# Kernel optimization log

Measured on AMD Instinct MI355X. Metric: run time of the kernel, lower is better.

The kernel has to match this reference:

```python
import jax, jax.numpy as jnp
import numpy as np

D_MODEL = 1024
NUM_HEADS = 16
HEAD_DIM = D_MODEL // NUM_HEADS
BATCH = 2048


def setup_inputs() -> dict:
    key = jax.random.key(0)
    ks = jax.random.split(key, 11)
    s = 1.0 / np.sqrt(D_MODEL)
    inp = {
        "q": jax.random.normal(ks[0], (BATCH, D_MODEL), jnp.float32),
        "k": jax.random.normal(ks[1], (BATCH, D_MODEL), jnp.float32),
        "v": jax.random.normal(ks[2], (BATCH, D_MODEL), jnp.float32),
        "Wq": jax.random.normal(ks[3], (D_MODEL, D_MODEL), jnp.float32) * s,
        "bq": jnp.zeros((D_MODEL,), jnp.float32),
        "Wk": jax.random.normal(ks[4], (D_MODEL, D_MODEL), jnp.float32) * s,
        "bk": jnp.zeros((D_MODEL,), jnp.float32),
        "Wv": jax.random.normal(ks[5], (D_MODEL, D_MODEL), jnp.float32) * s,
        "bv": jnp.zeros((D_MODEL,), jnp.float32),
        "Wo": jax.random.normal(ks[6], (D_MODEL, D_MODEL), jnp.float32) * s,
        "bo": jnp.zeros((D_MODEL,), jnp.float32),
    }
    return inp


def reference(q, k, v, Wq, bq, Wk, bk, Wv, bv, Wo, bo):
    b = q.shape[0]
    # linear projections (torch Linear: x @ W.T + b)
    qh = (q @ Wq.T + bq).reshape(b, NUM_HEADS, HEAD_DIM).transpose(1, 0, 2)  # (h, b, dh)
    kh = (k @ Wk.T + bk).reshape(b, NUM_HEADS, HEAD_DIM).transpose(1, 0, 2)  # (h, b, dh)
    # attention across the batch dimension: (h, b, b)
    scores = jnp.einsum('hid,hjd->hij', qh, kh) / jnp.sqrt(jnp.float32(HEAD_DIM))
    attn = jax.nn.softmax(scores, axis=-1)
    # pool_method == 'mean': v stays full-width, mean over heads
    vp = v @ Wv.T + bv                               # (b, d_model)
    out = jnp.einsum('hij,jd->hid', attn, vp)        # (h, b, d_model)
    out = out.mean(axis=0)                           # (b, d_model)
    out = out @ Wo.T + bo
    return out
```

## Files before the change

### kernel.cpp

```cpp
#include <hip/hip_runtime.h>
#include <hip/hip_bf16.h>
#include <stdint.h>

#define D_MODEL 1024
#define NUM_HEADS 16
#define HEAD_DIM 64
#define BATCH 2048

typedef unsigned short u16;
typedef __bf16 bf16x8 __attribute__((ext_vector_type(8)));
typedef float f32x4 __attribute__((ext_vector_type(4)));
typedef u16 u16x8 __attribute__((ext_vector_type(8)));

typedef __attribute__((address_space(1))) void gv_t;
typedef __attribute__((address_space(3))) void lv_t;

__device__ __forceinline__ u16 f2bf(float f) {
    uint32_t u = __builtin_bit_cast(uint32_t, f);
    return (u16)((u + 0x7fffu + ((u >> 16) & 1u)) >> 16);
}
__device__ __forceinline__ f32x4 fzero4() { f32x4 v = {0.f, 0.f, 0.f, 0.f}; return v; }

template<int N> __device__ __forceinline__ void waitv() {
    if constexpr (N == 0) asm volatile("s_waitcnt vmcnt(0)" ::: "memory");
    else if constexpr (N == 2) asm volatile("s_waitcnt vmcnt(2)" ::: "memory");
    else if constexpr (N == 4) asm volatile("s_waitcnt vmcnt(4)" ::: "memory");
    else if constexpr (N == 6) asm volatile("s_waitcnt vmcnt(6)" ::: "memory");
}
#define BAR() do { __builtin_amdgcn_s_barrier(); __builtin_amdgcn_sched_barrier(0); } while (0)

struct Conv7 {
    const float* src[7];
    u16* dst[7];
    int n[7];
};

__global__ __launch_bounds__(256) void convert_kernel(Conv7 a) {
    const int y = blockIdx.y;
    const int n = a.n[y];
    const long base = (long)(blockIdx.x * 256 + threadIdx.x) * 8;
    if (base >= n) return;
    const float* s = a.src[y] + base;
    const float4 f0 = *(const float4*)s;
    const float4 f1 = *(const float4*)(s + 4);
    u16x8 o;
    o[0] = f2bf(f0.x); o[1] = f2bf(f0.y); o[2] = f2bf(f0.z); o[3] = f2bf(f0.w);
    o[4] = f2bf(f1.x); o[5] = f2bf(f1.y); o[6] = f2bf(f1.z); o[7] = f2bf(f1.w);
    *(u16x8*)(a.dst[y] + base) = o;
}

struct G3 {
    const u16* A[3];
    const u16* Bt[3];
    const float* bias[3];
    void* C[3];
    int trans[3];
    int ldc[3];
};

__global__ __launch_bounds__(256, 3) void proj128_kernel(G3 g, int K) {
    __shared__ __align__(16) u16 As[3][128 * 32];
    __shared__ __align__(16) u16 Bs[3][128 * 32];
    const int z = blockIdx.z;
    const u16* __restrict__ A = g.A[z];
    const u16* __restrict__ Bt = g.Bt[z];
    const int tid = threadIdx.x, lane = tid & 63, wid = tid >> 6;
    const int l15 = lane & 15, l4 = lane >> 4;
    const int wr = wid >> 1, wc = wid & 1;
    const size_t brow = blockIdx.x, bcol = blockIdx.y;
    const int trow = tid >> 2;
    const int cswz = ((tid & 3) ^ (trow & 3)) * 8;
    const int sa = l15 & 3;

    const u16* Ag = A + (brow * 128 + trow) * (size_t)K + cswz;
    const u16* Bg = Bt + (bcol * 128 + trow) * (size_t)K + cswz;

    f32x4 acc[4][4];
#pragma unroll
    for (int m = 0; m < 4; m++)
#pragma unroll
        for (int n = 0; n < 4; n++) acc[m][n] = fzero4();

#define STGP(bi, k0) do { \
        __builtin_amdgcn_global_load_lds((gv_t*)(Ag + (k0)), (lv_t*)(&As[bi][tid * 8]), 16, 0, 0); \
        __builtin_amdgcn_global_load_lds((gv_t*)(Ag + (size_t)64 * K + (k0)), (lv_t*)(&As[bi][tid * 8 + 2048]), 16, 0, 0); \
        __builtin_amdgcn_global_load_lds((gv_t*)(Bg + (k0)), (lv_t*)(&Bs[bi][tid * 8]), 16, 0, 0); \
        __builtin_amdgcn_global_load_lds((gv_t*)(Bg + (size_t)64 * K + (k0)), (lv_t*)(&Bs[bi][tid * 8 + 2048]), 16, 0, 0); \
    } while (0)

    const int NT = K / 32;
    STGP(0, 0);
    STGP(1, 32);
    int cur = 0, pf = 2;
    for (int t = 0; t < NT; ++t) {
        if (t + 1 < NT) waitv<4>(); else waitv<0>();
        BAR();
        bf16x8 a[4], b[4];
#pragma unroll
        for (int m = 0; m < 4; m++) {
            const int row = wr * 64 + m * 16 + l15;
            a[m] = *(const bf16x8*)&As[cur][row * 32 + ((l4 ^ sa) * 8)];
        }
#pragma unroll
        for (int n = 0; n < 4; n++) {
            const int row = wc * 64 + n * 16 + l15;
            b[n] = *(const bf16x8*)&Bs[cur][row * 32 + ((l4 ^ sa) * 8)];
        }
        if (t + 2 < NT) STGP(pf, (t + 2) * 32);
        __builtin_amdgcn_s_setprio(1);
#pragma unroll
        for (int m = 0; m < 4; m++)
#pragma unroll
            for (int n = 0; n < 4; n++)
                acc[m][n] = __builtin_amdgcn_mfma_f32_16x16x32_bf16(a[m], b[n], acc[m][n], 0, 0, 0);
        __builtin_amdgcn_s_setprio(0);
        cur = (cur == 2) ? 0 : cur + 1;
        pf = (pf == 2) ? 0 : pf + 1;
    }
#undef STGP

    const int trans = g.trans[z];
    const size_t ldc = g.ldc[z];
    const float* bias = g.bias[z];
#pragma unroll
    for (int m = 0; m < 4; m++)
#pragma unroll
        for (int n = 0; n < 4; n++) {
            const size_t col = bcol * 128 + wc * 64 + n * 16 + l15;
            const float bv = bias[col];
#pragma unroll
            for (int j = 0; j < 4; j++) {
                const size_t row = brow * 128 + wr * 64 + m * 16 + l4 * 4 + j;
                const float val = acc[m][n][j] + bv;
                const size_t idx = trans ? (col * ldc + row) : (row * ldc + col);
                ((u16*)g.C[z])[idx] = f2bf(val);
            }
        }
}

template<int OUT_BF16, int HAS_BIAS>
__global__ __launch_bounds__(256, 2) void gemm64(G3 g, int K) {
    __shared__ __align__(16) u16 As[3][128 * 64];
    __shared__ __align__(16) u16 Bs[3][64 * 64];
    const int z = blockIdx.z;
    const u16* __restrict__ A = g.A[z];
    const u16* __restrict__ Bt = g.Bt[z];
    const int tid = threadIdx.x, lane = tid & 63, wid = tid >> 6;
    const int l15 = lane & 15, l4 = lane >> 4;
    const int wr = wid >> 1, wc = wid & 1;
    const size_t brow = blockIdx.x, bcol = blockIdx.y;
    const int trow = tid >> 3;
    const int cswz = ((tid & 7) ^ (trow & 7)) * 8;
    const int sa = l15 & 7;

    const u16* Ag = A + (brow * 128 + trow) * (size_t)K + cswz;
    const u16* Bg = Bt + (bcol * 64 + trow) * (size_t)K + cswz;

    f32x4 acc[4][2];
#pragma unroll
    for (int m = 0; m < 4; m++)
#pragma unroll
        for (int n = 0; n < 2; n++) acc[m][n] = fzero4();

#define STG64(bi, k0) do { \
        __builtin_amdgcn_global_load_lds((gv_t*)(Ag + (k0)), (lv_t*)(&As[bi][tid * 8]), 16, 0, 0); \
        __builtin_amdgcn_global_load_lds((gv_t*)(Ag + (size_t)32 * K + (k0)), (lv_t*)(&As[bi][tid * 8 + 2048]), 16, 0, 0); \
        __builtin_amdgcn_global_load_lds((gv_t*)(Ag + (size_t)64 * K + (k0)), (lv_t*)(&As[bi][tid * 8 + 4096]), 16, 0, 0); \
        __builtin_amdgcn_global_load_lds((gv_t*)(Ag + (size_t)96 * K + (k0)), (lv_t*)(&As[bi][tid * 8 + 6144]), 16, 0, 0); \
        __builtin_amdgcn_global_load_lds((gv_t*)(Bg + (k0)), (lv_t*)(&Bs[bi][tid * 8]), 16, 0, 0); \
        __builtin_amdgcn_global_load_lds((gv_t*)(Bg + (size_t)32 * K + (k0)), (lv_t*)(&Bs[bi][tid * 8 + 2048]), 16, 0, 0); \
    } while (0)

    const int NT = K / 64;
    STG64(0, 0);
    STG64(1, 64);
    int cur = 0, pf = 2;
    for (int t = 0; t < NT; ++t) {
        if (t + 1 < NT) waitv<6>(); else waitv<0>();
        BAR();
        bf16x8 a[4][2], b[2][2];
#pragma unroll
        for (int m = 0; m < 4; m++)
#pragma unroll
            for (int kk = 0; kk < 2; kk++)
                a[m][kk] = *(const bf16x8*)&As[cur][(wr * 64 + m * 16 + l15) * 64 + (((kk * 4 + l4) ^ sa) * 8)];
#pragma unroll
        for (int n = 0; n < 2; n++)
#pragma unroll
            for (int kk = 0; kk < 2; kk++)
                b[n][kk] = *(const bf16x8*)&Bs[cur][(wc * 32 + n * 16 + l15) * 64 + (((kk * 4 + l4) ^ sa) * 8)];
        if (t + 2 < NT) STG64(pf, (t + 2) * 64);
        __builtin_amdgcn_s_setprio(1);
#pragma unroll
        for (int m = 0; m < 4; m++)
#pragma unroll
            for (int n = 0; n < 2; n++) {
                acc[m][n] = __builtin_amdgcn_mfma_f32_16x16x32_bf16(a[m][0], b[n][0], acc[m][n], 0, 0, 0);
                acc[m][n] = __builtin_amdgcn_mfma_f32_16x16x32_bf16(a[m][1], b[n][1], acc[m][n], 0, 0, 0);
            }
        __builtin_amdgcn_s_setprio(0);
        cur = (cur == 2) ? 0 : cur + 1;
        pf = (pf == 2) ? 0 : pf + 1;
    }
#undef STG64

    const int trans = g.trans[z];
    const size_t ldc = g.ldc[z];
    const float* bias = g.bias[z];
#pragma unroll
    for (int m = 0; m < 4; m++)
#pragma unroll
        for (int n = 0; n < 2; n++) {
            const size_t col = bcol * 64 + wc * 32 + n * 16 + l15;
            const float bv = HAS_BIAS ? bias[col] : 0.f;
#pragma unroll
            for (int j = 0; j < 4; j++) {
                const size_t row = brow * 128 + wr * 64 + m * 16 + l4 * 4 + j;
                const float val = acc[m][n][j] + bv;
                if (OUT_BF16) {
                    const size_t idx = trans ? (col * ldc + row) : (row * ldc + col);
                    ((u16*)g.C[z])[idx] = f2bf(val);
                } else {
                    ((float*)g.C[z])[row * ldc + col] = val;
                }
            }
        }
}

__global__ __launch_bounds__(256, 2) void rowsum_kernel(
    const u16* __restrict__ Q, const u16* __restrict__ Kb, float* __restrict__ inv)
{
    __shared__ __align__(16) u16 Qs[2][64 * 32];
    __shared__ __align__(16) u16 Ks[3][2][64 * 32];
    const int tid = threadIdx.x, lane = tid & 63, wid = tid >> 6;
    const int l15 = lane & 15, l4 = lane >> 4;
    const int h = blockIdx.y;
    const size_t r0 = (size_t)blockIdx.x * 64;
    const int srow = tid >> 2;
    const int scol = (tid & 3) * 8;

#define STGR(bi, it) do { \
        __builtin_amdgcn_global_load_lds( \
            (gv_t*)(Kb + ((size_t)(it) * 64 + srow) * D_MODEL + h * HEAD_DIM + scol), \
            (lv_t*)(Ks[bi][0] + tid * 8), 16, 0, 0); \
        __builtin_amdgcn_global_load_lds( \
            (gv_t*)(Kb + ((size_t)(it) * 64 + srow) * D_MODEL + h * HEAD_DIM + 32 + scol), \
            (lv_t*)(Ks[bi][1] + tid * 8), 16, 0, 0); \
    } while (0)

#pragma unroll
    for (int kk = 0; kk < 2; kk++)
        __builtin_amdgcn_global_load_lds(
            (gv_t*)(Q + (r0 + srow) * D_MODEL + h * HEAD_DIM + kk * 32 + scol),
            (lv_t*)(Qs[kk] + tid * 8), 16, 0, 0);
    STGR(0, 0);
    STGR(1, 1);
    waitv<4>();
    BAR();
    bf16x8 aq[2];
#pragma unroll
    for (int kk = 0; kk < 2; kk++)
        aq[kk] = *(const bf16x8*)&Qs[kk][(wid * 16 + l15) * 32 + l4 * 8];

    float psum[4] = {0.f, 0.f, 0.f, 0.f};
    const int NT = BATCH / 64;
    int cur = 0, pf = 2;
    for (int it = 0; it < NT; ++it) {
        if (it + 1 < NT) waitv<2>(); else waitv<0>();
        BAR();
        bf16x8 b0[4], b1[4];
#pragma unroll
        for (int n = 0; n < 4; n++) {
            b0[n] = *(const bf16x8*)&Ks[cur][0][(n * 16 + l15) * 32 + l4 * 8];
            b1[n] = *(const bf16x8*)&Ks[cur][1][(n * 16 + l15) * 32 + l4 * 8];
        }
        if (it + 2 < NT) STGR(pf, it + 2);
        __builtin_amdgcn_s_setprio(1);
        f32x4 s[4];
#pragma unroll
        for (int n = 0; n < 4; n++) {
            s[n] = fzero4();
            s[n] = __builtin_amdgcn_mfma_f32_16x16x32_bf16(aq[0], b0[n], s[n], 0, 0, 0);
            s[n] = __builtin_amdgcn_mfma_f32_16x16x32_bf16(aq[1], b1[n], s[n], 0, 0, 0);
        }
        __builtin_amdgcn_s_setprio(0);
#pragma unroll
        for (int n = 0; n < 4; n++)
#pragma unroll
            for (int j = 0; j < 4; j++) psum[j] += __expf(s[n][j] * 0.125f);
        cur = (cur == 2) ? 0 : cur + 1;
        pf = (pf == 2) ? 0 : pf + 1;
    }
#undef STGR
#pragma unroll
    for (int off = 8; off >= 1; off >>= 1)
#pragma unroll
        for (int j = 0; j < 4; j++) psum[j] += __shfl_xor(psum[j], off, 64);
    if (l15 == 0) {
#pragma unroll
        for (int j = 0; j < 4; j++)
            inv[(size_t)h * BATCH + r0 + wid * 16 + l4 * 4 + j] = 1.0f / (16.0f * psum[j]);
    }
}

__global__ __launch_bounds__(256, 2) void ameanu_kernel(
    const u16* __restrict__ Q, const u16* __restrict__ Kb,
    const float* __restrict__ inv, u16* __restrict__ Am,
    const u16* __restrict__ wob, const u16* __restrict__ VP, u16* __restrict__ Ut)
{
    __shared__ __align__(16) u16 As[3][128 * 64];
    __shared__ __align__(16) u16 Bs[3][64 * 64];
    const int tid = threadIdx.x, lane = tid & 63, wid = tid >> 6;
    const int l15 = lane & 15, l4 = lane >> 4;
    const int wr = wid >> 1, wc = wid & 1;
    const int bx = blockIdx.x, by = blockIdx.y;
    const int trow = tid >> 3;
    const int cswz = ((tid & 7) ^ (trow & 7)) * 8;
    const int sa = l15 & 7;

    if (by >= 32) {
        const size_t brow = bx >> 1;
        const size_t bcol = (size_t)(by - 32) * 2 + (bx & 1);
        const int K = D_MODEL;
        const u16* Ag = wob + (brow * 128 + trow) * (size_t)K + cswz;
        const u16* Bg = VP + (bcol * 64 + trow) * (size_t)K + cswz;

        f32x4 acc[4][2];
#pragma unroll
        for (int m = 0; m < 4; m++)
#pragma unroll
            for (int n = 0; n < 2; n++) acc[m][n] = fzero4();

#define STGU(bi, k0) do { \
        __builtin_amdgcn_global_load_lds((gv_t*)(Ag + (k0)), (lv_t*)(&As[bi][tid * 8]), 16, 0, 0); \
        __builtin_amdgcn_global_load_lds((gv_t*)(Ag + (size_t)32 * K + (k0)), (lv_t*)(&As[bi][tid * 8 + 2048]), 16, 0, 0); \
        __builtin_amdgcn_global_load_lds((gv_t*)(Ag + (size_t)64 * K + (k0)), (lv_t*)(&As[bi][tid * 8 + 4096]), 16, 0, 0); \
        __builtin_amdgcn_global_load_lds((gv_t*)(Ag + (size_t)96 * K + (k0)), (lv_t*)(&As[bi][tid * 8 + 6144]), 16, 0, 0); \
        __builtin_amdgcn_global_load_lds((gv_t*)(Bg + (k0)), (lv_t*)(&Bs[bi][tid * 8]), 16, 0, 0); \
        __builtin_amdgcn_global_load_lds((gv_t*)(Bg + (size_t)32 * K + (k0)), (lv_t*)(&Bs[bi][tid * 8 + 2048]), 16, 0, 0); \
    } while (0)

        const int NT = K / 64;
        STGU(0, 0);
        STGU(1, 64);
        int cur = 0, pf = 2;
        for (int t = 0; t < NT; ++t) {
            if (t + 1 < NT) waitv<6>(); else waitv<0>();
            BAR();
            bf16x8 a[4][2], b[2][2];
#pragma unroll
            for (int m = 0; m < 4; m++)
#pragma unroll
                for (int kk = 0; kk < 2; kk++)
                    a[m][kk] = *(const bf16x8*)&As[cur][(wr * 64 + m * 16 + l15) * 64 + (((kk * 4 + l4) ^ sa) * 8)];
#pragma unroll
            for (int n = 0; n < 2; n++)
#pragma unroll
                for (int kk = 0; kk < 2; kk++)
                    b[n][kk] = *(const bf16x8*)&Bs[cur][(wc * 32 + n * 16 + l15) * 64 + (((kk * 4 + l4) ^ sa) * 8)];
            if (t + 2 < NT) STGU(pf, (t + 2) * 64);
            __builtin_amdgcn_s_setprio(1);
#pragma unroll
            for (int m = 0; m < 4; m++)
#pragma unroll
                for (int n = 0; n < 2; n++) {
                    acc[m][n] = __builtin_amdgcn_mfma_f32_16x16x32_bf16(a[m][0], b[n][0], acc[m][n], 0, 0, 0);
                    acc[m][n] = __builtin_amdgcn_mfma_f32_16x16x32_bf16(a[m][1], b[n][1], acc[m][n], 0, 0, 0);
                }
            __builtin_amdgcn_s_setprio(0);
            cur = (cur == 2) ? 0 : cur + 1;
            pf = (pf == 2) ? 0 : pf + 1;
        }
#undef STGU

#pragma unroll
        for (int m = 0; m < 4; m++)
#pragma unroll
            for (int n = 0; n < 2; n++) {
                const size_t col = bcol * 64 + wc * 32 + n * 16 + l15;
#pragma unroll
                for (int j = 0; j < 4; j++) {
                    const size_t row = brow * 128 + wr * 64 + m * 16 + l4 * 4 + j;
                    Ut[row * (size_t)BATCH + col] = f2bf(acc[m][n][j]);
                }
            }
        return;
    }

    const size_t brow = bx, bcol = by;
    const u16* Ag = Q + (brow * 128 + trow) * (size_t)D_MODEL + cswz;
    const u16* Bg = Kb + (bcol * 64 + trow) * (size_t)D_MODEL + cswz;

#define STGM(bi, k0) do { \
        __builtin_amdgcn_global_load_lds((gv_t*)(Ag + (k0)), (lv_t*)(&As[bi][tid * 8]), 16, 0, 0); \
        __builtin_amdgcn_global_load_lds((gv_t*)(Ag + (size_t)32 * D_MODEL + (k0)), (lv_t*)(&As[bi][tid * 8 + 2048]), 16, 0, 0); \
        __builtin_amdgcn_global_load_lds((gv_t*)(Ag + (size_t)64 * D_MODEL + (k0)), (lv_t*)(&As[bi][tid * 8 + 4096]), 16, 0, 0); \
        __builtin_amdgcn_global_load_lds((gv_t*)(Ag + (size_t)96 * D_MODEL + (k0)), (lv_t*)(&As[bi][tid * 8 + 6144]), 16, 0, 0); \
        __builtin_amdgcn_global_load_lds((gv_t*)(Bg + (k0)), (lv_t*)(&Bs[bi][tid * 8]), 16, 0, 0); \
        __builtin_amdgcn_global_load_lds((gv_t*)(Bg + (size_t)32 * D_MODEL + (k0)), (lv_t*)(&Bs[bi][tid * 8 + 2048]), 16, 0, 0); \
    } while (0)

    float accA[4][2][4] = {};
    STGM(0, 0);
    STGM(1, 64);
    int cur = 0, pf = 2;
    const float SC = 0.125f * 1.44269504088896341f;

    for (int h = 0; h < NUM_HEADS; h++) {
        if (h + 1 < NUM_HEADS) waitv<6>(); else waitv<0>();
        BAR();
        bf16x8 a[4][2], b[2][2];
#pragma unroll
        for (int m = 0; m < 4; m++)
#pragma unroll
            for (int kk = 0; kk < 2; kk++)
                a[m][kk] = *(const bf16x8*)&As[cur][(wr * 64 + m * 16 + l15) * 64 + (((kk * 4 + l4) ^ sa) * 8)];
#pragma unroll
        for (int n = 0; n < 2; n++)
#pragma unroll
            for (int kk = 0; kk < 2; kk++)
                b[n][kk] = *(const bf16x8*)&Bs[cur][(wc * 32 + n * 16 + l15) * 64 + (((kk * 4 + l4) ^ sa) * 8)];
        if (h + 2 < NUM_HEADS) STGM(pf, (h + 2) * 64);
        __builtin_amdgcn_s_setprio(1);
        f32x4 acc[4][2];
#pragma unroll
        for (int m = 0; m < 4; m++)
#pragma unroll
            for (int n = 0; n < 2; n++) {
                acc[m][n] = fzero4();
                acc[m][n] = __builtin_amdgcn_mfma_f32_16x16x32_bf16(a[m][0], b[n][0], acc[m][n], 0, 0, 0);
                acc[m][n] = __builtin_amdgcn_mfma_f32_16x16x32_bf16(a[m][1], b[n][1], acc[m][n], 0, 0, 0);
            }
        __builtin_amdgcn_s_setprio(0);
#pragma unroll
        for (int m = 0; m < 4; m++) {
            const f32x4 iv = *(const f32x4*)&inv[(size_t)h * BATCH + brow * 128 + wr * 64 + m * 16 + l4 * 4];
#pragma unroll
            for (int n = 0; n < 2; n++)
#pragma unroll
                for (int j = 0; j < 4; j++)
                    accA[m][n][j] += exp2f(acc[m][n][j] * SC) * iv[j];
        }
        cur = (cur == 2) ? 0 : cur + 1;
        pf = (pf == 2) ? 0 : pf + 1;
    }
#undef STGM

#pragma unroll
    for (int m = 0; m < 4; m++)
#pragma unroll
        for (int n = 0; n < 2; n++)
#pragma unroll
            for (int j = 0; j < 4; j++) {
                const size_t row = brow * 128 + wr * 64 + m * 16 + l4 * 4 + j;
                const size_t col = bcol * 64 + wc * 32 + n * 16 + l15;
                Am[row * (size_t)BATCH + col] = f2bf(accA[m][n][j]);
            }
}

extern "C" void kernel_launch(void* const* d_in, const int* in_sizes, int n_in,
                              void* d_out, int out_size, void* d_ws, size_t ws_size,
                              hipStream_t stream)
{
    const float* q  = (const float*)d_in[0];
    const float* k  = (const float*)d_in[1];
    const float* v  = (const float*)d_in[2];
    const float* Wq = (const float*)d_in[3];
    const float* bq = (const float*)d_in[4];
    const float* Wk = (const float*)d_in[5];
    const float* bk = (const float*)d_in[6];
    const float* Wv = (const float*)d_in[7];
    const float* bv = (const float*)d_in[8];
    const float* Wo = (const float*)d_in[9];
    const float* bo = (const float*)d_in[10];
    float* out = (float*)d_out;

    char* p = (char*)d_ws;
    u16* qb  = (u16*)p; p += (size_t)BATCH * D_MODEL * 2;
    u16* kb  = (u16*)p; p += (size_t)BATCH * D_MODEL * 2;
    u16* vb  = (u16*)p; p += (size_t)BATCH * D_MODEL * 2;
    u16* wqb = (u16*)p; p += (size_t)D_MODEL * D_MODEL * 2;
    u16* wkb = (u16*)p; p += (size_t)D_MODEL * D_MODEL * 2;
    u16* wvb = (u16*)p; p += (size_t)D_MODEL * D_MODEL * 2;
    u16* wob = (u16*)p; p += (size_t)D_MODEL * D_MODEL * 2;
    u16* Qb  = (u16*)p; p += (size_t)BATCH * D_MODEL * 2;
    u16* Kp  = (u16*)p; p += (size_t)BATCH * D_MODEL * 2;
    u16* VP  = (u16*)p; p += (size_t)BATCH * D_MODEL * 2;
    u16* Am  = (u16*)p; p += (size_t)BATCH * BATCH * 2;
    u16* Ut  = (u16*)p; p += (size_t)D_MODEL * BATCH * 2;
    float* inv = (float*)p;

    Conv7 ca;
    ca.src[0] = q;  ca.dst[0] = qb;  ca.n[0] = BATCH * D_MODEL;
    ca.src[1] = k;  ca.dst[1] = kb;  ca.n[1] = BATCH * D_MODEL;
    ca.src[2] = v;  ca.dst[2] = vb;  ca.n[2] = BATCH * D_MODEL;
    ca.src[3] = Wq; ca.dst[3] = wqb; ca.n[3] = D_MODEL * D_MODEL;
    ca.src[4] = Wk; ca.dst[4] = wkb; ca.n[4] = D_MODEL * D_MODEL;
    ca.src[5] = Wv; ca.dst[5] = wvb; ca.n[5] = D_MODEL * D_MODEL;
    ca.src[6] = Wo; ca.dst[6] = wob; ca.n[6] = D_MODEL * D_MODEL;
    convert_kernel<<<dim3(1024, 7), 256, 0, stream>>>(ca);

    G3 pr;
    pr.A[0] = qb; pr.Bt[0] = wqb; pr.bias[0] = bq; pr.C[0] = Qb; pr.trans[0] = 0; pr.ldc[0] = D_MODEL;
    pr.A[1] = kb; pr.Bt[1] = wkb; pr.bias[1] = bk; pr.C[1] = Kp; pr.trans[1] = 0; pr.ldc[1] = D_MODEL;
    pr.A[2] = vb; pr.Bt[2] = wvb; pr.bias[2] = bv; pr.C[2] = VP; pr.trans[2] = 0; pr.ldc[2] = D_MODEL;
    proj128_kernel<<<dim3(16, 8, 3), 256, 0, stream>>>(pr, D_MODEL);

    rowsum_kernel<<<dim3(BATCH / 64, NUM_HEADS), 256, 0, stream>>>(Qb, Kp, inv);

    ameanu_kernel<<<dim3(16, 48), 256, 0, stream>>>(Qb, Kp, inv, Am, wob, VP, Ut);

    G3 go;
    go.A[0] = Am; go.Bt[0] = Ut; go.bias[0] = bo; go.C[0] = out; go.trans[0] = 0; go.ldc[0] = D_MODEL;
    go.A[1] = go.A[0]; go.Bt[1] = go.Bt[0]; go.bias[1] = go.bias[0]; go.C[1] = go.C[0]; go.trans[1] = 0; go.ldc[1] = D_MODEL;
    go.A[2] = go.A[0]; go.Bt[2] = go.Bt[0]; go.bias[2] = go.bias[0]; go.C[2] = go.C[0]; go.trans[2] = 0; go.ldc[2] = D_MODEL;
    gemm64<0, 1><<<dim3(16, 16, 1), 256, 0, stream>>>(go, BATCH);
}
```

Baseline: 106.4 us.

## Split-K the final GEMM into two halves with a separate reduction kernel

The final Am×Ut GEMM (K=2048) is split along K into two 1024-long halves computed by separate blocks (grid z=2), each writing fp32 partials to workspace. A new elementwise kernel sums the two partials and adds the output bias. This doubles the block count from 256 to 512 to fill more CUs on a small grid. In exchange it adds 16 MB of partial writes and reads plus an extra kernel launch.

```diff
diff --git a/kernel.cpp b/kernel.cpp
--- a/kernel.cpp
+++ b/kernel.cpp
@@ -138,23 +138,24 @@
         }
 }
 
-template<int OUT_BF16, int HAS_BIAS>
-__global__ __launch_bounds__(256, 2) void gemm64(G3 g, int K) {
+__global__ __launch_bounds__(256, 2) void final_sk(
+    const u16* __restrict__ A, const u16* __restrict__ Bt, float* __restrict__ S)
+{
     __shared__ __align__(16) u16 As[3][128 * 64];
     __shared__ __align__(16) u16 Bs[3][64 * 64];
-    const int z = blockIdx.z;
-    const u16* __restrict__ A = g.A[z];
-    const u16* __restrict__ Bt = g.Bt[z];
     const int tid = threadIdx.x, lane = tid & 63, wid = tid >> 6;
     const int l15 = lane & 15, l4 = lane >> 4;
     const int wr = wid >> 1, wc = wid & 1;
     const size_t brow = blockIdx.x, bcol = blockIdx.y;
+    const int koff = blockIdx.z * 1024;
+    float* C = S + (size_t)blockIdx.z * BATCH * D_MODEL;
     const int trow = tid >> 3;
     const int cswz = ((tid & 7) ^ (trow & 7)) * 8;
     const int sa = l15 & 7;
-
-    const u16* Ag = A + (brow * 128 + trow) * (size_t)K + cswz;
-    const u16* Bg = Bt + (bcol * 64 + trow) * (size_t)K + cswz;
+    const size_t LDK = BATCH;
+
+    const u16* Ag = A + (brow * 128 + trow) * LDK + koff + cswz;
+    const u16* Bg = Bt + (bcol * 64 + trow) * LDK + koff + cswz;
 
     f32x4 acc[4][2];
 #pragma unroll
@@ -162,18 +163,18 @@
 #pragma unroll
         for (int n = 0; n < 2; n++) acc[m][n] = fzero4();
 
-#define STG64(bi, k0) do { \
+#define STGF(bi, k0) do { \
         __builtin_amdgcn_global_load_lds((gv_t*)(Ag + (k0)), (lv_t*)(&As[bi][tid * 8]), 16, 0, 0); \
-        __builtin_amdgcn_global_load_lds((gv_t*)(Ag + (size_t)32 * K + (k0)), (lv_t*)(&As[bi][tid * 8 + 2048]), 16, 0, 0); \
-        __builtin_amdgcn_global_load_lds((gv_t*)(Ag + (size_t)64 * K + (k0)), (lv_t*)(&As[bi][tid * 8 + 4096]), 16, 0, 0); \
-        __builtin_amdgcn_global_load_lds((gv_t*)(Ag + (size_t)96 * K + (k0)), (lv_t*)(&As[bi][tid * 8 + 6144]), 16, 0, 0); \
+        __builtin_amdgcn_global_load_lds((gv_t*)(Ag + (size_t)32 * LDK + (k0)), (lv_t*)(&As[bi][tid * 8 + 2048]), 16, 0, 0); \
+        __builtin_amdgcn_global_load_lds((gv_t*)(Ag + (size_t)64 * LDK + (k0)), (lv_t*)(&As[bi][tid * 8 + 4096]), 16, 0, 0); \
+        __builtin_amdgcn_global_load_lds((gv_t*)(Ag + (size_t)96 * LDK + (k0)), (lv_t*)(&As[bi][tid * 8 + 6144]), 16, 0, 0); \
         __builtin_amdgcn_global_load_lds((gv_t*)(Bg + (k0)), (lv_t*)(&Bs[bi][tid * 8]), 16, 0, 0); \
-        __builtin_amdgcn_global_load_lds((gv_t*)(Bg + (size_t)32 * K + (k0)), (lv_t*)(&Bs[bi][tid * 8 + 2048]), 16, 0, 0); \
+        __builtin_amdgcn_global_load_lds((gv_t*)(Bg + (size_t)32 * LDK + (k0)), (lv_t*)(&Bs[bi][tid * 8 + 2048]), 16, 0, 0); \
     } while (0)
 
-    const int NT = K / 64;
-    STG64(0, 0);
-    STG64(1, 64);
+    const int NT = 1024 / 64;
+    STGF(0, 0);
+    STGF(1, 64);
     int cur = 0, pf = 2;
     for (int t = 0; t < NT; ++t) {
         if (t + 1 < NT) waitv<6>(); else waitv<0>();
@@ -189,7 +190,7 @@
 #pragma unroll
             for (int kk = 0; kk < 2; kk++)
                 b[n][kk] = *(const bf16x8*)&Bs[cur][(wc * 32 + n * 16 + l15) * 64 + (((kk * 4 + l4) ^ sa) * 8)];
-        if (t + 2 < NT) STG64(pf, (t + 2) * 64);
+        if (t + 2 < NT) STGF(pf, (t + 2) * 64);
         __builtin_amdgcn_s_setprio(1);
 #pragma unroll
         for (int m = 0; m < 4; m++)
@@ -202,29 +203,35 @@
         cur = (cur == 2) ? 0 : cur + 1;
         pf = (pf == 2) ? 0 : pf + 1;
     }
-#undef STG64
-
-    const int trans = g.trans[z];
-    const size_t ldc = g.ldc[z];
-    const float* bias = g.bias[z];
+#undef STGF
+
 #pragma unroll
     for (int m = 0; m < 4; m++)
 #pragma unroll
         for (int n = 0; n < 2; n++) {
             const size_t col = bcol * 64 + wc * 32 + n * 16 + l15;
-            const float bv = HAS_BIAS ? bias[col] : 0.f;
 #pragma unroll
             for (int j = 0; j < 4; j++) {
                 const size_t row = brow * 128 + wr * 64 + m * 16 + l4 * 4 + j;
-                const float val = acc[m][n][j] + bv;
-                if (OUT_BF16) {
-                    const size_t idx = trans ? (col * ldc + row) : (row * ldc + col);
-                    ((u16*)g.C[z])[idx] = f2bf(val);
-                } else {
-                    ((float*)g.C[z])[row * ldc + col] = val;
-                }
+                C[row * (size_t)D_MODEL + col] = acc[m][n][j];
             }
         }
+}
+
+__global__ __launch_bounds__(256) void reduce_kernel(
+    const float* __restrict__ s0, const float* __restrict__ s1,
+    const float* __restrict__ bo, float* __restrict__ out)
+{
+    const size_t idx = ((size_t)blockIdx.x * 256 + threadIdx.x) * 4;
+    const float4 a = *(const float4*)&s0[idx];
+    const float4 b = *(const float4*)&s1[idx];
+    const float4 bias = *(const float4*)&bo[idx & (D_MODEL - 1)];
+    float4 r;
+    r.x = a.x + b.x + bias.x;
+    r.y = a.y + b.y + bias.y;
+    r.z = a.z + b.z + bias.z;
+    r.w = a.w + b.w + bias.w;
+    *(float4*)&out[idx] = r;
 }
 
 __global__ __launch_bounds__(256, 2) void rowsum_kernel(
@@ -488,7 +495,9 @@
     u16* VP  = (u16*)p; p += (size_t)BATCH * D_MODEL * 2;
     u16* Am  = (u16*)p; p += (size_t)BATCH * BATCH * 2;
     u16* Ut  = (u16*)p; p += (size_t)D_MODEL * BATCH * 2;
-    float* inv = (float*)p;
+    float* inv = (float*)p; p += (size_t)NUM_HEADS * BATCH * 4;
+    float* s0 = (float*)p; p += (size_t)BATCH * D_MODEL * 4;
+    float* s1 = (float*)p;
 
     Conv7 ca;
     ca.src[0] = q;  ca.dst[0] = qb;  ca.n[0] = BATCH * D_MODEL;
@@ -510,9 +519,7 @@
 
     ameanu_kernel<<<dim3(16, 48), 256, 0, stream>>>(Qb, Kp, inv, Am, wob, VP, Ut);
 
-    G3 go;
-    go.A[0] = Am; go.Bt[0] = Ut; go.bias[0] = bo; go.C[0] = out; go.trans[0] = 0; go.ldc[0] = D_MODEL;
-    go.A[1] = go.A[0]; go.Bt[1] = go.Bt[0]; go.bias[1] = go.bias[0]; go.C[1] = go.C[0]; go.trans[1] = 0; go.ldc[1] = D_MODEL;
-    go.A[2] = go.A[0]; go.Bt[2] = go.Bt[0]; go.bias[2] = go.bias[0]; go.C[2] = go.C[0]; go.trans[2] = 0; go.ldc[2] = D_MODEL;
-    gemm64<0, 1><<<dim3(16, 16, 1), 256, 0, stream>>>(go, BATCH);
-}
+    final_sk<<<dim3(16, 16, 2), 256, 0, stream>>>(Am, Ut, s0);
+
+    reduce_kernel<<<dim3(BATCH * D_MODEL / 1024), 256, 0, stream>>>(s0, s1, bo, out);
+}
```

Result: no change. 106.9 us (+0.5%).
